# Optimization experiments

Hardware: AMD Instinct MI355X
Metric: run time of the kernel (lower is better)

Reference implementation:

```python
import jax, jax.numpy as jnp
import numpy as np

EPS_S = 1e-06
EPS_R = 1e-06

def _gaussian_masks(mu, logsx, logsy, rho, H, W, dtype):
    # coordinate grid in [-1,1], grid[h,w] = (x, y)
    ys = jnp.linspace(-1.0, 1.0, H, dtype=dtype)
    xs = jnp.linspace(-1.0, 1.0, W, dtype=dtype)
    Y, X = jnp.meshgrid(ys, xs, indexing='ij')  # [H,W]
    sx = jnp.exp(logsx)[:, None, None] + EPS_S   # [n,1,1]
    sy = jnp.exp(logsy)[:, None, None] + EPS_S
    r = jnp.tanh(rho)[:, None, None]
    xc = (X[None] - mu[:, 0, None, None]) / sx   # [n,H,W]
    yc = (Y[None] - mu[:, 1, None, None]) / sy
    A = xc ** 2 + yc ** 2 - 2.0 * r * xc * yc
    denom = 2.0 * (1.0 - r ** 2 + EPS_R)
    return jnp.exp(-A / denom)                   # [n,H,W]

def setup_inputs() -> dict:
    key = jax.random.key(0)
    ks = jax.random.split(key, 6)
    B, C, H, W, n = 32, 256, 36, 64, 4096
    feat = jax.random.normal(ks[0], (B, C, H, W), dtype=jnp.float32)
    mu = jax.random.uniform(ks[1], (n, 2), dtype=jnp.float32) * 2.0 - 1.0
    logsx = jnp.zeros((n,), dtype=jnp.float32)
    logsy = jnp.zeros((n,), dtype=jnp.float32)
    rho = jnp.zeros((n,), dtype=jnp.float32)
    weight = jax.random.normal(ks[5], (n, C), dtype=jnp.float32) * 0.01
    return {"feat": feat, "mu": mu, "logsx": logsx, "logsy": logsy, "rho": rho, "weight": weight}

def reference(feat, mu, logsx, logsy, rho, weight):
    B, C, H, W = feat.shape
    G = _gaussian_masks(mu, logsx, logsy, rho, H, W, feat.dtype)  # [n,H,W]
    # pooled[b,n,c] = sum_{h,w} feat[b,c,h,w] * G[n,h,w]  (batched GEMM)
    pooled = jnp.einsum('bchw,nhw->bnc', feat, G)
    out = jnp.einsum('bnc,nc->bn', pooled, weight.astype(feat.dtype))
    return out
```

## Files before the change

kernel.cpp:

```cpp
#include <hip/hip_runtime.h>
#include <hip/hip_bf16.h>

#define P_HW   2304
#define NG     4096
#define NCOL   8192
#define KDIM   P_HW
#define NT     72

typedef __bf16 bf16x8 __attribute__((ext_vector_type(8)));
typedef float  f32x4  __attribute__((ext_vector_type(4)));

__device__ __forceinline__ unsigned short f2bf(float f) {
    union { float f; unsigned int u; } x; x.f = f;
    unsigned int r = x.u + 0x7FFFu + ((x.u >> 16) & 1u);
    return (unsigned short)(r >> 16);
}

__global__ __launch_bounds__(256) void prep_kernel(
    const float* __restrict__ feat,
    const float* __restrict__ mu,
    const float* __restrict__ logsx,
    const float* __restrict__ logsy,
    const float* __restrict__ rho,
    unsigned short* __restrict__ F,
    unsigned short* __restrict__ G,
    float* __restrict__ out) {
    const int bid = blockIdx.x;
    const int tid = threadIdx.x;
    if (bid < 9216) {
        const size_t i = ((size_t)bid * 256 + tid) * 8;
        const float4 v0 = *(const float4*)(feat + i);
        const float4 v1 = *(const float4*)(feat + i + 4);
        union { unsigned short s[8]; uint4 q; } o;
        o.s[0] = f2bf(v0.x); o.s[1] = f2bf(v0.y); o.s[2] = f2bf(v0.z); o.s[3] = f2bf(v0.w);
        o.s[4] = f2bf(v1.x); o.s[5] = f2bf(v1.y); o.s[6] = f2bf(v1.z); o.s[7] = f2bf(v1.w);
        *(uint4*)(F + i) = o.q;
    } else if (bid < 13312) {
        const int n = bid - 9216;
        const float mux = mu[2 * n], muy = mu[2 * n + 1];
        const float sx = __expf(logsx[n]) + 1e-6f;
        const float sy = __expf(logsy[n]) + 1e-6f;
        const float r  = tanhf(rho[n]);
        const float inv_den = 1.0f / (2.0f * (1.0f - r * r + 1e-6f));
        const float isx = 1.0f / sx, isy = 1.0f / sy;
        for (int base = tid * 8; base < P_HW; base += 2048) {
            const int h = base >> 6, w0 = base & 63;
            const float Y  = -1.0f + (float)h * (2.0f / 35.0f);
            const float yc = (Y - muy) * isy;
            union { unsigned short s[8]; uint4 q; } o;
#pragma unroll
            for (int j = 0; j < 8; ++j) {
                const float X  = -1.0f + (float)(w0 + j) * (2.0f / 63.0f);
                const float xc = (X - mux) * isx;
                const float A  = xc * xc + yc * yc - 2.0f * r * xc * yc;
                o.s[j] = f2bf(__expf(-A * inv_den));
            }
            *(uint4*)&G[(size_t)n * P_HW + base] = o.q;
        }
    } else {
        const size_t i = ((size_t)(bid - 13312) * 256 + tid) * 8;
        const float4 z = {0.f, 0.f, 0.f, 0.f};
        *(float4*)(out + i)     = z;
        *(float4*)(out + i + 4) = z;
    }
}

__device__ __forceinline__ void async16(const void* g, void* l) {
    __builtin_amdgcn_global_load_lds(
        (__attribute__((address_space(1))) void*)(unsigned long long)g,
        (__attribute__((address_space(3))) void*)(unsigned int)(unsigned long long)l,
        16, 0, 0);
}

__global__ __launch_bounds__(512, 2) void gemm_fused(
    const unsigned short* __restrict__ G,
    const unsigned short* __restrict__ F,
    const float* __restrict__ weight,
    float* __restrict__ out)
{
    __shared__ __align__(16) unsigned short lds[4 * 16384];

    const int tid  = threadIdx.x;
    const int lane = tid & 63;
    const int wid  = tid >> 6;
    const int wr   = wid >> 2;
    const int wc   = wid & 3;
    const int quad = lane >> 4, m = lane & 15;

    const int rowBase = blockIdx.y * 256;
    const int colBase = blockIdx.x * 256;

    const int rA = tid >> 2;
    const int cA = (tid & 3) ^ ((tid >> 3) & 3);
    const unsigned short* pA = G + (size_t)(rowBase + rA) * KDIM + cA * 8;
    const unsigned short* pB = F + (size_t)(colBase + rA) * KDIM + cA * 8;

    const int sw   = (quad ^ ((m >> 1) & 3)) * 8;
    const int aoff = (wr * 128 + m) * 32 + sw;
    const int boff = (wc * 64  + m) * 32 + sw;

    f32x4 acc[8][4];
#pragma unroll
    for (int i = 0; i < 8; ++i)
#pragma unroll
        for (int j = 0; j < 4; ++j)
            acc[i][j] = (f32x4){0.f, 0.f, 0.f, 0.f};

#pragma unroll
    for (int t = 0; t < 3; ++t) {
        const int bo = t * 16384;
        async16(pA + t * 32,                  &lds[bo + tid * 8]);
        async16(pA + t * 32 + 128 * KDIM,     &lds[bo + 4096 + tid * 8]);
        async16(pB + t * 32,                  &lds[bo + 8192 + tid * 8]);
        async16(pB + t * 32 + 128 * KDIM,     &lds[bo + 12288 + tid * 8]);
    }
    asm volatile("s_waitcnt vmcnt(8)" ::: "memory");
    __builtin_amdgcn_s_barrier();
    asm volatile("" ::: "memory");

    for (int tt = 0; tt < NT; tt += 4) {
#pragma unroll
        for (int u = 0; u < 4; ++u) {
            const int t   = tt + u;
            const int bo  = u * 16384;
            const int wbo = ((u + 3) & 3) * 16384;
            int w = t + 3;
            if (w >= NT) w -= NT;
            const unsigned short* pAw = pA + w * 32;
            const unsigned short* pBw = pB + w * 32;

            async16(pAw,              &lds[wbo + tid * 8]);
            async16(pAw + 128 * KDIM, &lds[wbo + 4096 + tid * 8]);
            async16(pBw,              &lds[wbo + 8192 + tid * 8]);
            async16(pBw + 128 * KDIM, &lds[wbo + 12288 + tid * 8]);

            bf16x8 a[8], b[4];
#pragma unroll
            for (int j = 0; j < 4; ++j)
                b[j] = *(const bf16x8*)&lds[bo + 8192 + boff + j * 512];
#pragma unroll
            for (int i = 0; i < 8; ++i)
                a[i] = *(const bf16x8*)&lds[bo + aoff + i * 512];

            __builtin_amdgcn_s_setprio(1);
#pragma unroll
            for (int i = 0; i < 8; ++i)
#pragma unroll
                for (int j = 0; j < 4; ++j)
                    acc[i][j] = __builtin_amdgcn_mfma_f32_16x16x32_bf16(a[i], b[j], acc[i][j], 0, 0, 0);
            __builtin_amdgcn_s_setprio(0);

            asm volatile("s_waitcnt vmcnt(8)" ::: "memory");
            __builtin_amdgcn_s_barrier();
            asm volatile("" ::: "memory");
        }
    }

    asm volatile("s_waitcnt vmcnt(0)" ::: "memory");
    __syncthreads();

    float* red = (float*)lds;
    const int cwbase = wc * 64 + m;
#pragma unroll
    for (int i = 0; i < 8; ++i) {
#pragma unroll
        for (int reg = 0; reg < 4; ++reg) {
            const int nloc = wr * 128 + i * 16 + quad * 4 + reg;
            const float* wrow = weight + (size_t)(rowBase + nloc) * 256 + cwbase;
            float s = 0.f;
#pragma unroll
            for (int j = 0; j < 4; ++j)
                s += acc[i][j][reg] * wrow[j * 16];
            s += __shfl_xor(s, 1);
            s += __shfl_xor(s, 2);
            s += __shfl_xor(s, 4);
            s += __shfl_xor(s, 8);
            if (m == 0)
                red[wc * 256 + nloc] = s;
        }
    }
    __syncthreads();
    if (tid < 256) {
        const float s = red[tid] + red[256 + tid] + red[512 + tid] + red[768 + tid];
        out[(size_t)blockIdx.x * NG + rowBase + tid] = s;
    }
}

extern "C" void kernel_launch(void* const* d_in, const int* in_sizes, int n_in,
                              void* d_out, int out_size, void* d_ws, size_t ws_size,
                              hipStream_t stream) {
    const float* feat   = (const float*)d_in[0];
    const float* mu     = (const float*)d_in[1];
    const float* logsx  = (const float*)d_in[2];
    const float* logsy  = (const float*)d_in[3];
    const float* rho    = (const float*)d_in[4];
    const float* weight = (const float*)d_in[5];
    float* out = (float*)d_out;

    unsigned short* Gbuf = (unsigned short*)d_ws;
    unsigned short* Fbuf = Gbuf + (size_t)NG * P_HW;

    hipLaunchKernelGGL(prep_kernel, dim3(13376), dim3(256), 0, stream,
                       feat, mu, logsx, logsy, rho, Fbuf, Gbuf, out);

    hipLaunchKernelGGL(gemm_fused, dim3(NCOL / 256, NG / 256), dim3(512), 0, stream,
                       Gbuf, Fbuf, weight, out);
}
```

Measured before the change: 270.3 us.

## Restructure GEMM main loop into 8-phase ping-pong schedule with K=64 tiles

Changes the K tile from 32 to 64 with a double-buffered LDS layout and a new 8-column XOR swizzle. Each K step is split into four quadrant MFMA phases, and global-to-LDS loads are interleaved between barriers in the style of HipKittens/ping-pong GEMM scheduling. The aim is to overlap LDS reads, async global loads and MFMA issue more finely and to cut barrier count per unit of work. The cost is a more intricate synchronization pattern with more barriers per tile, and correctness depends on subtle vmcnt accounting.

```diff
diff --git a/kernel.cpp b/kernel.cpp
--- a/kernel.cpp
+++ b/kernel.cpp
@@ -5,7 +5,7 @@
 #define NG     4096
 #define NCOL   8192
 #define KDIM   P_HW
-#define NT     72
+#define NKT    36
 
 typedef __bf16 bf16x8 __attribute__((ext_vector_type(8)));
 typedef float  f32x4  __attribute__((ext_vector_type(4)));
@@ -78,7 +78,7 @@
     const float* __restrict__ weight,
     float* __restrict__ out)
 {
-    __shared__ __align__(16) unsigned short lds[4 * 16384];
+    __shared__ __align__(16) unsigned short lds[2 * 32768];
 
     const int tid  = threadIdx.x;
     const int lane = tid & 63;
@@ -90,14 +90,20 @@
     const int rowBase = blockIdx.y * 256;
     const int colBase = blockIdx.x * 256;
 
-    const int rA = tid >> 2;
-    const int cA = (tid & 3) ^ ((tid >> 3) & 3);
-    const unsigned short* pA = G + (size_t)(rowBase + rA) * KDIM + cA * 8;
-    const unsigned short* pB = F + (size_t)(colBase + rA) * KDIM + cA * 8;
-
-    const int sw   = (quad ^ ((m >> 1) & 3)) * 8;
-    const int aoff = (wr * 128 + m) * 32 + sw;
-    const int boff = (wc * 64  + m) * 32 + sw;
+    const int rS = tid >> 3;
+    const int cS = (tid & 7) ^ (rS & 7);
+    const unsigned short* pA = G + (size_t)(rowBase + rS) * KDIM + cS * 8;
+    const unsigned short* pB = F + (size_t)(colBase + rS) * KDIM + cS * 8;
+
+#define STG_A(buf, q, kt) async16(pA + (q) * 64 * KDIM + (kt) * 64, \
+        &lds[(buf) * 32768 + (q) * 4096 + tid * 8])
+#define STG_B(buf, q, kt) async16(pB + (q) * 64 * KDIM + (kt) * 64, \
+        &lds[(buf) * 32768 + 16384 + (q) * 4096 + tid * 8])
+
+    const int arow = (wr * 128 + m) * 64;
+    const int brow = (wc * 64  + m) * 64;
+    const int cs0  = ((quad)     ^ (m & 7)) * 8;
+    const int cs1  = ((4 + quad) ^ (m & 7)) * 8;
 
     f32x4 acc[8][4];
 #pragma unroll
@@ -106,54 +112,119 @@
         for (int j = 0; j < 4; ++j)
             acc[i][j] = (f32x4){0.f, 0.f, 0.f, 0.f};
 
-#pragma unroll
-    for (int t = 0; t < 3; ++t) {
-        const int bo = t * 16384;
-        async16(pA + t * 32,                  &lds[bo + tid * 8]);
-        async16(pA + t * 32 + 128 * KDIM,     &lds[bo + 4096 + tid * 8]);
-        async16(pB + t * 32,                  &lds[bo + 8192 + tid * 8]);
-        async16(pB + t * 32 + 128 * KDIM,     &lds[bo + 12288 + tid * 8]);
-    }
-    asm volatile("s_waitcnt vmcnt(8)" ::: "memory");
+    STG_A(0, 0, 0); STG_A(0, 1, 0); STG_A(0, 2, 0); STG_A(0, 3, 0);
+    STG_B(0, 0, 0); STG_B(0, 1, 0); STG_B(0, 2, 0); STG_B(0, 3, 0);
+    STG_A(1, 0, 1); STG_A(1, 2, 1);
+    STG_B(1, 0, 1); STG_B(1, 1, 1);
+    STG_A(1, 1, 1); STG_A(1, 3, 1);
+    asm volatile("s_waitcnt vmcnt(6)" ::: "memory");
     __builtin_amdgcn_s_barrier();
-    asm volatile("" ::: "memory");
-
-    for (int tt = 0; tt < NT; tt += 4) {
-#pragma unroll
-        for (int u = 0; u < 4; ++u) {
-            const int t   = tt + u;
-            const int bo  = u * 16384;
-            const int wbo = ((u + 3) & 3) * 16384;
-            int w = t + 3;
-            if (w >= NT) w -= NT;
-            const unsigned short* pAw = pA + w * 32;
-            const unsigned short* pBw = pB + w * 32;
-
-            async16(pAw,              &lds[wbo + tid * 8]);
-            async16(pAw + 128 * KDIM, &lds[wbo + 4096 + tid * 8]);
-            async16(pBw,              &lds[wbo + 8192 + tid * 8]);
-            async16(pBw + 128 * KDIM, &lds[wbo + 12288 + tid * 8]);
-
-            bf16x8 a[8], b[4];
-#pragma unroll
-            for (int j = 0; j < 4; ++j)
-                b[j] = *(const bf16x8*)&lds[bo + 8192 + boff + j * 512];
-#pragma unroll
-            for (int i = 0; i < 8; ++i)
-                a[i] = *(const bf16x8*)&lds[bo + aoff + i * 512];
-
-            __builtin_amdgcn_s_setprio(1);
-#pragma unroll
-            for (int i = 0; i < 8; ++i)
-#pragma unroll
-                for (int j = 0; j < 4; ++j)
-                    acc[i][j] = __builtin_amdgcn_mfma_f32_16x16x32_bf16(a[i], b[j], acc[i][j], 0, 0, 0);
-            __builtin_amdgcn_s_setprio(0);
-
-            asm volatile("s_waitcnt vmcnt(8)" ::: "memory");
-            __builtin_amdgcn_s_barrier();
-            asm volatile("" ::: "memory");
-        }
+
+#define MFMA_Q(IOFF, JOFF, AX, BX)                                         \
+    __builtin_amdgcn_s_setprio(1);                                         \
+    _Pragma("unroll")                                                      \
+    for (int fi = 0; fi < 4; ++fi)                                         \
+        _Pragma("unroll")                                                  \
+        for (int fj = 0; fj < 2; ++fj)                                     \
+            _Pragma("unroll")                                              \
+            for (int kk = 0; kk < 2; ++kk)                                 \
+                acc[fi + IOFF][fj + JOFF] =                                \
+                    __builtin_amdgcn_mfma_f32_16x16x32_bf16(               \
+                        AX[fi][kk], BX[fj][kk], acc[fi + IOFF][fj + JOFF], \
+                        0, 0, 0);                                          \
+    __builtin_amdgcn_s_setprio(0);
+
+#define BARRIER_IN()  __builtin_amdgcn_s_barrier();                        \
+                      asm volatile("s_waitcnt lgkmcnt(0)" ::: "memory");
+#define BARRIER_OUT() __builtin_amdgcn_s_barrier();
+
+    for (int it = 0; it < NKT / 2; ++it) {
+        const int t = 2 * it;
+        int k2 = t + 2; if (k2 >= NKT) k2 -= NKT;
+        int k3 = t + 3; if (k3 >= NKT) k3 -= NKT;
+        bf16x8 a[4][2], blo[2][2], bhi[2][2];
+
+#pragma unroll
+        for (int fi = 0; fi < 4; ++fi) {
+            a[fi][0] = *(const bf16x8*)&lds[arow + fi * 1024 + cs0];
+            a[fi][1] = *(const bf16x8*)&lds[arow + fi * 1024 + cs1];
+        }
+#pragma unroll
+        for (int fj = 0; fj < 2; ++fj) {
+            blo[fj][0] = *(const bf16x8*)&lds[16384 + brow + fj * 1024 + cs0];
+            blo[fj][1] = *(const bf16x8*)&lds[16384 + brow + fj * 1024 + cs1];
+        }
+        STG_B(1, 2, t + 1); STG_B(1, 3, t + 1);
+        BARRIER_IN();
+        MFMA_Q(0, 0, a, blo);
+        BARRIER_OUT();
+
+#pragma unroll
+        for (int fj = 0; fj < 2; ++fj) {
+            bhi[fj][0] = *(const bf16x8*)&lds[16384 + brow + 2048 + fj * 1024 + cs0];
+            bhi[fj][1] = *(const bf16x8*)&lds[16384 + brow + 2048 + fj * 1024 + cs1];
+        }
+        STG_A(0, 0, k2); STG_A(0, 2, k2);
+        BARRIER_IN();
+        MFMA_Q(0, 2, a, bhi);
+        BARRIER_OUT();
+
+#pragma unroll
+        for (int fi = 0; fi < 4; ++fi) {
+            a[fi][0] = *(const bf16x8*)&lds[arow + 4096 + fi * 1024 + cs0];
+            a[fi][1] = *(const bf16x8*)&lds[arow + 4096 + fi * 1024 + cs1];
+        }
+        STG_B(0, 0, k2); STG_B(0, 2, k2);
+        BARRIER_IN();
+        MFMA_Q(4, 2, a, bhi);
+        BARRIER_OUT();
+
+        STG_A(0, 1, k2); STG_A(0, 3, k2);
+        asm volatile("s_waitcnt vmcnt(6)" ::: "memory");
+        BARRIER_IN();
+        MFMA_Q(4, 0, a, blo);
+        BARRIER_OUT();
+
+#pragma unroll
+        for (int fi = 0; fi < 4; ++fi) {
+            a[fi][0] = *(const bf16x8*)&lds[32768 + arow + fi * 1024 + cs0];
+            a[fi][1] = *(const bf16x8*)&lds[32768 + arow + fi * 1024 + cs1];
+        }
+#pragma unroll
+        for (int fj = 0; fj < 2; ++fj) {
+            blo[fj][0] = *(const bf16x8*)&lds[32768 + 16384 + brow + fj * 1024 + cs0];
+            blo[fj][1] = *(const bf16x8*)&lds[32768 + 16384 + brow + fj * 1024 + cs1];
+        }
+        STG_B(0, 1, k2); STG_B(0, 3, k2);
+        BARRIER_IN();
+        MFMA_Q(0, 0, a, blo);
+        BARRIER_OUT();
+
+#pragma unroll
+        for (int fj = 0; fj < 2; ++fj) {
+            bhi[fj][0] = *(const bf16x8*)&lds[32768 + 16384 + brow + 2048 + fj * 1024 + cs0];
+            bhi[fj][1] = *(const bf16x8*)&lds[32768 + 16384 + brow + 2048 + fj * 1024 + cs1];
+        }
+        STG_A(1, 0, k3); STG_A(1, 2, k3);
+        BARRIER_IN();
+        MFMA_Q(0, 2, a, bhi);
+        BARRIER_OUT();
+
+#pragma unroll
+        for (int fi = 0; fi < 4; ++fi) {
+            a[fi][0] = *(const bf16x8*)&lds[32768 + arow + 4096 + fi * 1024 + cs0];
+            a[fi][1] = *(const bf16x8*)&lds[32768 + arow + 4096 + fi * 1024 + cs1];
+        }
+        STG_B(1, 0, k3); STG_B(1, 1, k3);
+        BARRIER_IN();
+        MFMA_Q(4, 2, a, bhi);
+        BARRIER_OUT();
+
+        STG_A(1, 1, k3); STG_A(1, 3, k3);
+        asm volatile("s_waitcnt vmcnt(6)" ::: "memory");
+        BARRIER_IN();
+        MFMA_Q(4, 0, a, blo);
+        BARRIER_OUT();
     }
 
     asm volatile("s_waitcnt vmcnt(0)" ::: "memory");
```

Result: no change. 269.9 us (-0.2%).

## Generate Gaussian mask tiles inside GEMM mainloop instead of loading precomputed G

Applied to the files above, without the earlier changes.

Removes G precomputation from the prep kernel and computes each A tile of Gaussian masks directly into LDS inside the GEMM loop, one stage ahead, while F tiles are still loaded asynchronously three stages ahead. This eliminates writing and repeatedly reading the bf16 G buffer from global memory. The cost is redundant exp/ALU work in every column block and extra LDS store traffic competing with MFMA issue in the mainloop.

```diff
diff --git a/kernel.cpp b/kernel.cpp
--- a/kernel.cpp
+++ b/kernel.cpp
@@ -18,51 +18,14 @@
 
 __global__ __launch_bounds__(256) void prep_kernel(
     const float* __restrict__ feat,
-    const float* __restrict__ mu,
-    const float* __restrict__ logsx,
-    const float* __restrict__ logsy,
-    const float* __restrict__ rho,
-    unsigned short* __restrict__ F,
-    unsigned short* __restrict__ G,
-    float* __restrict__ out) {
-    const int bid = blockIdx.x;
-    const int tid = threadIdx.x;
-    if (bid < 9216) {
-        const size_t i = ((size_t)bid * 256 + tid) * 8;
-        const float4 v0 = *(const float4*)(feat + i);
-        const float4 v1 = *(const float4*)(feat + i + 4);
-        union { unsigned short s[8]; uint4 q; } o;
-        o.s[0] = f2bf(v0.x); o.s[1] = f2bf(v0.y); o.s[2] = f2bf(v0.z); o.s[3] = f2bf(v0.w);
-        o.s[4] = f2bf(v1.x); o.s[5] = f2bf(v1.y); o.s[6] = f2bf(v1.z); o.s[7] = f2bf(v1.w);
-        *(uint4*)(F + i) = o.q;
-    } else if (bid < 13312) {
-        const int n = bid - 9216;
-        const float mux = mu[2 * n], muy = mu[2 * n + 1];
-        const float sx = __expf(logsx[n]) + 1e-6f;
-        const float sy = __expf(logsy[n]) + 1e-6f;
-        const float r  = tanhf(rho[n]);
-        const float inv_den = 1.0f / (2.0f * (1.0f - r * r + 1e-6f));
-        const float isx = 1.0f / sx, isy = 1.0f / sy;
-        for (int base = tid * 8; base < P_HW; base += 2048) {
-            const int h = base >> 6, w0 = base & 63;
-            const float Y  = -1.0f + (float)h * (2.0f / 35.0f);
-            const float yc = (Y - muy) * isy;
-            union { unsigned short s[8]; uint4 q; } o;
-#pragma unroll
-            for (int j = 0; j < 8; ++j) {
-                const float X  = -1.0f + (float)(w0 + j) * (2.0f / 63.0f);
-                const float xc = (X - mux) * isx;
-                const float A  = xc * xc + yc * yc - 2.0f * r * xc * yc;
-                o.s[j] = f2bf(__expf(-A * inv_den));
-            }
-            *(uint4*)&G[(size_t)n * P_HW + base] = o.q;
-        }
-    } else {
-        const size_t i = ((size_t)(bid - 13312) * 256 + tid) * 8;
-        const float4 z = {0.f, 0.f, 0.f, 0.f};
-        *(float4*)(out + i)     = z;
-        *(float4*)(out + i + 4) = z;
-    }
+    unsigned short* __restrict__ F) {
+    const size_t i = ((size_t)blockIdx.x * 256 + threadIdx.x) * 8;
+    const float4 v0 = *(const float4*)(feat + i);
+    const float4 v1 = *(const float4*)(feat + i + 4);
+    union { unsigned short s[8]; uint4 q; } o;
+    o.s[0] = f2bf(v0.x); o.s[1] = f2bf(v0.y); o.s[2] = f2bf(v0.z); o.s[3] = f2bf(v0.w);
+    o.s[4] = f2bf(v1.x); o.s[5] = f2bf(v1.y); o.s[6] = f2bf(v1.z); o.s[7] = f2bf(v1.w);
+    *(uint4*)(F + i) = o.q;
 }
 
 __device__ __forceinline__ void async16(const void* g, void* l) {
@@ -73,8 +36,11 @@
 }
 
 __global__ __launch_bounds__(512, 2) void gemm_fused(
-    const unsigned short* __restrict__ G,
     const unsigned short* __restrict__ F,
+    const float* __restrict__ mu,
+    const float* __restrict__ logsx,
+    const float* __restrict__ logsy,
+    const float* __restrict__ rho,
     const float* __restrict__ weight,
     float* __restrict__ out)
 {
@@ -92,8 +58,40 @@
 
     const int rA = tid >> 2;
     const int cA = (tid & 3) ^ ((tid >> 3) & 3);
-    const unsigned short* pA = G + (size_t)(rowBase + rA) * KDIM + cA * 8;
     const unsigned short* pB = F + (size_t)(colBase + rA) * KDIM + cA * 8;
+
+    float mux[2], muy[2], isx[2], isy[2], rr[2], inv[2];
+#pragma unroll
+    for (int i = 0; i < 2; ++i) {
+        const int n = rowBase + (tid >> 2) + i * 128;
+        mux[i] = mu[2 * n]; muy[i] = mu[2 * n + 1];
+        isx[i] = 1.0f / (__expf(logsx[n]) + 1e-6f);
+        isy[i] = 1.0f / (__expf(logsy[n]) + 1e-6f);
+        const float r = tanhf(rho[n]);
+        rr[i]  = r;
+        inv[i] = 1.0f / (2.0f * (1.0f - r * r + 1e-6f));
+    }
+
+#define GEN_A(KT, DST)                                                     \
+    {                                                                      \
+        const int   k0 = (KT) * 32;                                        \
+        const float Yt = -1.0f + (float)(k0 >> 6) * (2.0f / 35.0f);        \
+        const int   wb = (k0 & 32) + cA * 8;                               \
+        _Pragma("unroll")                                                  \
+        for (int i = 0; i < 2; ++i) {                                      \
+            const float yc = (Yt - muy[i]) * isy[i];                       \
+            union { unsigned short s[8]; uint4 q; } o;                     \
+            _Pragma("unroll")                                              \
+            for (int j = 0; j < 8; ++j) {                                  \
+                const float X  = -1.0f + (float)(wb + j) * (2.0f / 63.0f); \
+                const float xc = (X - mux[i]) * isx[i];                    \
+                const float A  = xc * xc + yc * yc                         \
+                                 - 2.0f * rr[i] * xc * yc;                 \
+                o.s[j] = f2bf(__expf(-A * inv[i]));                        \
+            }                                                              \
+            *(uint4*)&lds[(DST) + i * 4096 + tid * 8] = o.q;               \
+        }                                                                  \
+    }
 
     const int sw   = (quad ^ ((m >> 1) & 3)) * 8;
     const int aoff = (wr * 128 + m) * 32 + sw;
@@ -106,33 +104,30 @@
         for (int j = 0; j < 4; ++j)
             acc[i][j] = (f32x4){0.f, 0.f, 0.f, 0.f};
 
-#pragma unroll
-    for (int t = 0; t < 3; ++t) {
-        const int bo = t * 16384;
-        async16(pA + t * 32,                  &lds[bo + tid * 8]);
-        async16(pA + t * 32 + 128 * KDIM,     &lds[bo + 4096 + tid * 8]);
-        async16(pB + t * 32,                  &lds[bo + 8192 + tid * 8]);
-        async16(pB + t * 32 + 128 * KDIM,     &lds[bo + 12288 + tid * 8]);
-    }
-    asm volatile("s_waitcnt vmcnt(8)" ::: "memory");
+    GEN_A(0, 0);
+#pragma unroll
+    for (int t2 = 0; t2 < 3; ++t2) {
+        async16(pB + t2 * 32,              &lds[t2 * 16384 + 8192  + tid * 8]);
+        async16(pB + t2 * 32 + 128 * KDIM, &lds[t2 * 16384 + 12288 + tid * 8]);
+    }
+    asm volatile("s_waitcnt vmcnt(4) lgkmcnt(0)" ::: "memory");
     __builtin_amdgcn_s_barrier();
     asm volatile("" ::: "memory");
 
     for (int tt = 0; tt < NT; tt += 4) {
 #pragma unroll
         for (int u = 0; u < 4; ++u) {
-            const int t   = tt + u;
-            const int bo  = u * 16384;
-            const int wbo = ((u + 3) & 3) * 16384;
-            int w = t + 3;
-            if (w >= NT) w -= NT;
-            const unsigned short* pAw = pA + w * 32;
-            const unsigned short* pBw = pB + w * 32;
-
-            async16(pAw,              &lds[wbo + tid * 8]);
-            async16(pAw + 128 * KDIM, &lds[wbo + 4096 + tid * 8]);
-            async16(pBw,              &lds[wbo + 8192 + tid * 8]);
-            async16(pBw + 128 * KDIM, &lds[wbo + 12288 + tid * 8]);
+            const int t    = tt + u;
+            const int bo   = u * 16384;
+            const int wAbo = ((u + 1) & 3) * 16384;
+            const int wBbo = ((u + 3) & 3) * 16384;
+            int wA = t + 1; if (wA >= NT) wA -= NT;
+            int wB = t + 3; if (wB >= NT) wB -= NT;
+            const unsigned short* pBw = pB + wB * 32;
+
+            async16(pBw,              &lds[wBbo + 8192  + tid * 8]);
+            async16(pBw + 128 * KDIM, &lds[wBbo + 12288 + tid * 8]);
+            GEN_A(wA, wAbo);
 
             bf16x8 a[8], b[4];
 #pragma unroll
@@ -150,13 +145,13 @@
                     acc[i][j] = __builtin_amdgcn_mfma_f32_16x16x32_bf16(a[i], b[j], acc[i][j], 0, 0, 0);
             __builtin_amdgcn_s_setprio(0);
 
-            asm volatile("s_waitcnt vmcnt(8)" ::: "memory");
+            asm volatile("s_waitcnt vmcnt(4) lgkmcnt(0)" ::: "memory");
             __builtin_amdgcn_s_barrier();
             asm volatile("" ::: "memory");
         }
     }
 
-    asm volatile("s_waitcnt vmcnt(0)" ::: "memory");
+    asm volatile("s_waitcnt vmcnt(0) lgkmcnt(0)" ::: "memory");
     __syncthreads();
 
     float* red = (float*)lds;
@@ -197,12 +192,10 @@
     const float* weight = (const float*)d_in[5];
     float* out = (float*)d_out;
 
-    unsigned short* Gbuf = (unsigned short*)d_ws;
-    unsigned short* Fbuf = Gbuf + (size_t)NG * P_HW;
-
-    hipLaunchKernelGGL(prep_kernel, dim3(13376), dim3(256), 0, stream,
-                       feat, mu, logsx, logsy, rho, Fbuf, Gbuf, out);
+    unsigned short* Fbuf = (unsigned short*)d_ws;
+
+    hipLaunchKernelGGL(prep_kernel, dim3(9216), dim3(256), 0, stream, feat, Fbuf);
 
     hipLaunchKernelGGL(gemm_fused, dim3(NCOL / 256, NG / 256), dim3(512), 0, stream,
-                       Gbuf, Fbuf, weight, out);
-}
+                       Fbuf, mu, logsx, logsy, rho, weight, out);
+}
```

Measured after the change: 860.3 us. 3.18x slower.
